# Optimization experiments

Measured on AMD Instinct MI355X. Metric: run time of the kernel, lower is better.

Reference implementation:

```python
import jax, jax.numpy as jnp
import numpy as np

EPS = 1e-5

def _layernorm(x, gamma, beta):
    mu = jnp.mean(x, axis=-1, keepdims=True)
    var = jnp.mean(jnp.square(x - mu), axis=-1, keepdims=True)
    return (x - mu) * jax.lax.rsqrt(var + EPS) * gamma + beta

def setup_inputs() -> dict:
    key = jax.random.key(0)
    kx, kw = jax.random.split(key)
    N, D, BIT = 65536, 1024, 64
    X = jax.random.normal(kx, (N, D), dtype=jnp.float32)
    # xavier_uniform with gain=0.5 for weight [BIT, D]
    limit = 0.5 * np.sqrt(6.0 / (D + BIT))
    W = jax.random.uniform(kw, (BIT, D), minval=-limit, maxval=limit, dtype=jnp.float32)
    b = jnp.zeros((BIT,), dtype=jnp.float32)
    ln1_g = jnp.ones((D,), dtype=jnp.float32)
    ln1_b = jnp.zeros((D,), dtype=jnp.float32)
    ln2_g = jnp.ones((BIT,), dtype=jnp.float32)
    ln2_b = jnp.zeros((BIT,), dtype=jnp.float32)
    return {"X": X, "W": W, "b": b, "ln1_g": ln1_g, "ln1_b": ln1_b, "ln2_g": ln2_g, "ln2_b": ln2_b}

def reference(X, W, b, ln1_g, ln1_b, ln2_g, ln2_b):
    # LayerNorm -> Linear -> LayerNorm
    xn = _layernorm(X, ln1_g, ln1_b)                       # [N, D]
    logits = jnp.einsum('nd,bd->nb', xn, W) + b            # [N, BIT]
    logits = _layernorm(logits, ln2_g, ln2_b)
    # mean-center over batch, tanh, sign-binarize
    logits = logits - jnp.mean(logits, axis=0, keepdims=True)
    H = jnp.tanh(0.5 * logits)
    B = jnp.where(H >= 0.0, jnp.int8(1), jnp.int8(-1))
    return H, B
```

## Files before the change

kernel.cpp:

```cpp
#include <hip/hip_runtime.h>
#include <stdint.h>

#define N_ROWS 65536
#define D_IN   1024
#define NBIT   64
#define LN_EPS 1e-5f

typedef __attribute__((ext_vector_type(8))) _Float16 f16x8;
typedef __attribute__((ext_vector_type(4))) float f32x4;

__device__ __forceinline__ void gload_lds16(const void* g, void* l) {
    __builtin_amdgcn_global_load_lds(
        (const __attribute__((address_space(1))) uint32_t*)g,
        (__attribute__((address_space(3))) uint32_t*)l, 16, 0, 0);
}

__device__ __forceinline__ f32x4 ntload4(const float* p) {
    return __builtin_nontemporal_load((const f32x4*)p);
}

__device__ __forceinline__ f32x4 mfma16(f16x8 a, f16x8 b, f32x4 c) {
    return __builtin_amdgcn_mfma_f32_16x16x32_f16(a, b, c, 0, 0, 0);
}

__device__ __forceinline__ void do_tstep(f32x4 x0, f32x4 x1,
        const _Float16* bhp, f32x4* acc_h, f32x4* acc_m, f32x4* acc_ll,
        float& sum, float& sumsq) {
    float xs[8] = {x0[0], x0[1], x0[2], x0[3], x1[0], x1[1], x1[2], x1[3]};
    f16x8 ahi, alo;
#pragma unroll
    for (int j = 0; j < 8; ++j) {
        float xv = xs[j];
        sum += xv;
        sumsq = fmaf(xv, xv, sumsq);
        _Float16 h = (_Float16)xv;
        ahi[j] = h;
        alo[j] = (_Float16)((xv - (float)h) * 2048.0f);
    }
#pragma unroll
    for (int nt = 0; nt < 4; ++nt) {
        f16x8 bh = *(const f16x8*)(bhp + nt * 512);
        f16x8 bl = *(const f16x8*)(bhp + 4096 + nt * 512);
        acc_h[nt]  = mfma16(ahi, bh, acc_h[nt]);
        acc_m[nt]  = mfma16(ahi, bl, acc_m[nt]);
        acc_m[nt]  = mfma16(alo, bh, acc_m[nt]);
        acc_ll[nt] = mfma16(alo, bl, acc_ll[nt]);
    }
}

__global__ void prep_kernel(const float* __restrict__ W, const float* __restrict__ bias,
                            const float* __restrict__ g1, const float* __restrict__ b1,
                            _Float16* __restrict__ whi, _Float16* __restrict__ wlo,
                            float* __restrict__ u, float* __restrict__ v) {
    int bit = blockIdx.x;
    int t   = threadIdx.x;
    int nt  = bit >> 4, bl = bit & 15;
    float su = 0.f, sv = 0.f;
    for (int d = t; d < D_IN; d += 256) {
        float w  = W[bit * D_IN + d];
        float gw = w * g1[d];
        su += gw;
        sv += w * b1[d];
        int kt = d >> 5, gg = (d >> 3) & 3, j = d & 7;
        size_t idx = (((size_t)(kt * 4 + nt)) * 64 + gg * 16 + bl) * 8 + j;
        _Float16 h = (_Float16)gw;
        whi[idx] = h;
        wlo[idx] = (_Float16)((gw - (float)h) * 2048.0f);
    }
    __shared__ float s1[256], s2[256];
    s1[t] = su; s2[t] = sv;
    __syncthreads();
    for (int off = 128; off > 0; off >>= 1) {
        if (t < off) { s1[t] += s1[t + off]; s2[t] += s2[t + off]; }
        __syncthreads();
    }
    if (t == 0) { u[bit] = s1[0]; v[bit] = s2[0] + bias[bit]; }
}

__global__ void __launch_bounds__(1024) main_kernel(
        const float* __restrict__ X,
        const _Float16* __restrict__ whi, const _Float16* __restrict__ wlo,
        const float* __restrict__ u, const float* __restrict__ v,
        const float* __restrict__ g2, const float* __restrict__ b2,
        float* __restrict__ L, float* __restrict__ P) {
    __shared__ _Float16 lw[2][8192];
    int tid  = threadIdx.x;
    int wid  = tid >> 6, lane = tid & 63;
    int g    = lane >> 4, r16 = lane & 15;
    int row_base = blockIdx.x * 256 + wid * 16;

    const float* xrow = X + (size_t)(row_base + r16) * D_IN + g * 8;

    const _Float16* gsrc = ((wid & 8) ? wlo : whi) + (wid & 7) * 512 + (size_t)lane * 8;
    const int ldst = ((wid & 8) ? 4096 : 0) + (wid & 7) * 512;

#define STAGEW(cc, buf) gload_lds16(gsrc + (size_t)(cc) * 4096, &lw[buf][ldst])

    f32x4 acc_h0[4], acc_h1[4], acc_m[4], acc_ll[4];
#pragma unroll
    for (int nt = 0; nt < 4; ++nt) {
        acc_h0[nt] = (f32x4){0.f, 0.f, 0.f, 0.f};
        acc_h1[nt] = (f32x4){0.f, 0.f, 0.f, 0.f};
        acc_m[nt]  = (f32x4){0.f, 0.f, 0.f, 0.f};
        acc_ll[nt] = (f32x4){0.f, 0.f, 0.f, 0.f};
    }
    float sum = 0.f, sumsq = 0.f;

    STAGEW(0, 0);
    __syncthreads();

    for (int c = 0; c < 16; ++c) {
        if (c < 15) STAGEW(c + 1, (c + 1) & 1);
        int t = c * 2;
        f32x4 x00 = ntload4(xrow + t * 32);
        f32x4 x01 = ntload4(xrow + t * 32 + 4);
        f32x4 x10 = ntload4(xrow + t * 32 + 32);
        f32x4 x11 = ntload4(xrow + t * 32 + 36);
        const _Float16* bhp = &lw[c & 1][0] + lane * 8;
        do_tstep(x00, x01, bhp,        acc_h0, acc_m, acc_ll, sum, sumsq);
        do_tstep(x10, x11, bhp + 2048, acc_h1, acc_m, acc_ll, sum, sumsq);
        __syncthreads();
    }

    sum   += __shfl_xor(sum, 16);   sum   += __shfl_xor(sum, 32);
    sumsq += __shfl_xor(sumsq, 16); sumsq += __shfl_xor(sumsq, 32);
    float mu   = sum * (1.f / 1024.f);
    float var  = sumsq * (1.f / 1024.f) - mu * mu;
    float rstd = rsqrtf(var + LN_EPS);

    float uv[4], vv[4], g2v[4], b2v[4];
#pragma unroll
    for (int nt = 0; nt < 4; ++nt) {
        int bitc = nt * 16 + r16;
        uv[nt] = u[bitc]; vv[nt] = v[bitc]; g2v[nt] = g2[bitc]; b2v[nt] = b2[bitc];
    }
    float mu_m[4], rs_m[4];
#pragma unroll
    for (int reg = 0; reg < 4; ++reg) {
        int m = g * 4 + reg;
        mu_m[reg] = __shfl(mu, m);
        rs_m[reg] = __shfl(rstd, m);
    }

    float lg[4][4];
#pragma unroll
    for (int nt = 0; nt < 4; ++nt)
#pragma unroll
        for (int reg = 0; reg < 4; ++reg) {
            float dot = (acc_h0[nt][reg] + acc_h1[nt][reg])
                      + acc_m[nt][reg] * (1.0f / 2048.0f)
                      + acc_ll[nt][reg] * (1.0f / 4194304.0f);
            lg[nt][reg] = rs_m[reg] * dot - rs_m[reg] * mu_m[reg] * uv[nt] + vv[nt];
        }

#pragma unroll
    for (int reg = 0; reg < 4; ++reg) {
        float s1 = lg[0][reg] + lg[1][reg] + lg[2][reg] + lg[3][reg];
        float s2 = lg[0][reg]*lg[0][reg] + lg[1][reg]*lg[1][reg]
                 + lg[2][reg]*lg[2][reg] + lg[3][reg]*lg[3][reg];
#pragma unroll
        for (int m = 1; m <= 8; m <<= 1) {
            s1 += __shfl_xor(s1, m);
            s2 += __shfl_xor(s2, m);
        }
        float mean = s1 * (1.f / 64.f);
        float va   = s2 * (1.f / 64.f) - mean * mean;
        float rs2  = rsqrtf(va + LN_EPS);
#pragma unroll
        for (int nt = 0; nt < 4; ++nt)
            lg[nt][reg] = (lg[nt][reg] - mean) * rs2 * g2v[nt] + b2v[nt];
    }

#pragma unroll
    for (int reg = 0; reg < 4; ++reg) {
        size_t row = (size_t)(row_base + g * 4 + reg);
#pragma unroll
        for (int nt = 0; nt < 4; ++nt)
            __builtin_nontemporal_store(lg[nt][reg], &L[row * 64 + nt * 16 + r16]);
    }

#pragma unroll
    for (int nt = 0; nt < 4; ++nt) {
        float cs = lg[nt][0] + lg[nt][1] + lg[nt][2] + lg[nt][3];
        cs += __shfl_xor(cs, 16);
        cs += __shfl_xor(cs, 32);
        if (g == 0)
            P[(size_t)(nt * 16 + r16) * 4096 + blockIdx.x * 16 + wid] = cs;
    }
#undef STAGEW
}

__global__ void reduce_kernel(const float* __restrict__ P, float* __restrict__ cm) {
    int bit = blockIdx.x, t = threadIdx.x;
    float s = 0.f;
    for (int p = t; p < 4096; p += 256) s += P[(size_t)bit * 4096 + p];
    __shared__ float sh[256];
    sh[t] = s;
    __syncthreads();
    for (int off = 128; off > 0; off >>= 1) {
        if (t < off) sh[t] += sh[t + off];
        __syncthreads();
    }
    if (t == 0) cm[bit] = sh[0] * (1.f / (float)N_ROWS);
}

__global__ void final_kernel(const float* __restrict__ L, const float* __restrict__ cm,
                             float* __restrict__ out) {
    __shared__ float cms[64];
    if (threadIdx.x < 64) cms[threadIdx.x] = cm[threadIdx.x];
    __syncthreads();
    const f32x4* L4 = (const f32x4*)L;
    f32x4* H4 = (f32x4*)out;
    f32x4* B4 = (f32x4*)(out + (size_t)N_ROWS * NBIT);
    int total = N_ROWS * NBIT / 4;
    for (int i = blockIdx.x * blockDim.x + threadIdx.x; i < total;
         i += gridDim.x * blockDim.x) {
        f32x4 x = __builtin_nontemporal_load(&L4[i]);
        int bb = (i & 15) * 4;
        f32x4 h, bo;
#pragma unroll
        for (int j = 0; j < 4; ++j) {
            h[j]  = tanhf(0.5f * (x[j] - cms[bb + j]));
            bo[j] = h[j] >= 0.f ? 1.f : -1.f;
        }
        __builtin_nontemporal_store(h, &H4[i]);
        __builtin_nontemporal_store(bo, &B4[i]);
    }
}

extern "C" void kernel_launch(void* const* d_in, const int* in_sizes, int n_in,
                              void* d_out, int out_size, void* d_ws, size_t ws_size,
                              hipStream_t stream) {
    (void)in_sizes; (void)n_in; (void)out_size; (void)ws_size;
    const float* X  = (const float*)d_in[0];
    const float* W  = (const float*)d_in[1];
    const float* bb = (const float*)d_in[2];
    const float* g1 = (const float*)d_in[3];
    const float* b1 = (const float*)d_in[4];
    const float* g2 = (const float*)d_in[5];
    const float* b2 = (const float*)d_in[6];

    char* ws = (char*)d_ws;
    _Float16* whi = (_Float16*)ws;
    _Float16* wlo = (_Float16*)(ws + 131072);
    float* u  = (float*)(ws + 262144);
    float* v  = (float*)(ws + 266240);
    float* P  = (float*)(ws + 270336);
    float* cm = (float*)(ws + 270336 + 64 * 4096 * 4);

    float* out = (float*)d_out;
    float* L   = out + (size_t)N_ROWS * NBIT;

    prep_kernel<<<64, 256, 0, stream>>>(W, bb, g1, b1, whi, wlo, u, v);
    main_kernel<<<256, 1024, 0, stream>>>(X, whi, wlo, u, v, g2, b2, L, P);
    reduce_kernel<<<64, 256, 0, stream>>>(P, cm);
    final_kernel<<<2048, 256, 0, stream>>>(L, cm, out);
}
```

Measured before the change: 100.6 us.

## Shrink main blocks to 256 threads, deepen K chunks, use fast tanh

The main kernel moves from 1024-thread blocks over 256 rows to 256-thread blocks over 64 rows, launched as 1024 blocks. Each K chunk now covers 128 columns, with the weight staging tile doubled and each wave issuing eight LDS loads per stage. Nontemporal loads and stores of X and L become ordinary cached accesses, so L may stay in cache for the final pass. The final kernel replaces tanhf with a cubic polynomial for small arguments and __expf otherwise, cutting transcendental cost at some accuracy loss near the switch point. The trade-off is that each block now re-stages the full weight matrix for a quarter as many rows.

Result: faster. 91.87 us (-8.6%).

```diff
diff --git a/kernel.cpp b/kernel.cpp
--- a/kernel.cpp
+++ b/kernel.cpp
@@ -13,10 +13,6 @@
     __builtin_amdgcn_global_load_lds(
         (const __attribute__((address_space(1))) uint32_t*)g,
         (__attribute__((address_space(3))) uint32_t*)l, 16, 0, 0);
-}
-
-__device__ __forceinline__ f32x4 ntload4(const float* p) {
-    return __builtin_nontemporal_load((const f32x4*)p);
 }
 
 __device__ __forceinline__ f32x4 mfma16(f16x8 a, f16x8 b, f32x4 c) {
@@ -40,7 +36,7 @@
 #pragma unroll
     for (int nt = 0; nt < 4; ++nt) {
         f16x8 bh = *(const f16x8*)(bhp + nt * 512);
-        f16x8 bl = *(const f16x8*)(bhp + 4096 + nt * 512);
+        f16x8 bl = *(const f16x8*)(bhp + 8192 + nt * 512);
         acc_h[nt]  = mfma16(ahi, bh, acc_h[nt]);
         acc_m[nt]  = mfma16(ahi, bl, acc_m[nt]);
         acc_m[nt]  = mfma16(alo, bh, acc_m[nt]);
@@ -77,24 +73,30 @@
     if (t == 0) { u[bit] = s1[0]; v[bit] = s2[0] + bias[bit]; }
 }
 
-__global__ void __launch_bounds__(1024) main_kernel(
+__global__ void __launch_bounds__(256) main_kernel(
         const float* __restrict__ X,
         const _Float16* __restrict__ whi, const _Float16* __restrict__ wlo,
         const float* __restrict__ u, const float* __restrict__ v,
         const float* __restrict__ g2, const float* __restrict__ b2,
         float* __restrict__ L, float* __restrict__ P) {
-    __shared__ _Float16 lw[2][8192];
+    __shared__ _Float16 lw[2][16384];
     int tid  = threadIdx.x;
     int wid  = tid >> 6, lane = tid & 63;
     int g    = lane >> 4, r16 = lane & 15;
-    int row_base = blockIdx.x * 256 + wid * 16;
+    int row_base = blockIdx.x * 64 + wid * 16;
 
     const float* xrow = X + (size_t)(row_base + r16) * D_IN + g * 8;
 
-    const _Float16* gsrc = ((wid & 8) ? wlo : whi) + (wid & 7) * 512 + (size_t)lane * 8;
-    const int ldst = ((wid & 8) ? 4096 : 0) + (wid & 7) * 512;
-
-#define STAGEW(cc, buf) gload_lds16(gsrc + (size_t)(cc) * 4096, &lw[buf][ldst])
+    const _Float16* gsrc = ((wid & 2) ? wlo : whi) + (wid & 1) * 4096 + (size_t)lane * 8;
+    const int ldst = ((wid & 2) ? 8192 : 0) + (wid & 1) * 4096;
+
+#define STAGEW(cc, buf) do {                                                  \
+        const _Float16* gs_ = gsrc + (size_t)(cc) * 8192;                     \
+        _Float16* ld_ = &lw[buf][ldst];                                       \
+        _Pragma("unroll")                                                     \
+        for (int r = 0; r < 8; ++r)                                           \
+            gload_lds16(gs_ + r * 512, ld_ + r * 512);                        \
+    } while (0)
 
     f32x4 acc_h0[4], acc_h1[4], acc_m[4], acc_ll[4];
 #pragma unroll
@@ -109,16 +111,21 @@
     STAGEW(0, 0);
     __syncthreads();
 
-    for (int c = 0; c < 16; ++c) {
-        if (c < 15) STAGEW(c + 1, (c + 1) & 1);
-        int t = c * 2;
-        f32x4 x00 = ntload4(xrow + t * 32);
-        f32x4 x01 = ntload4(xrow + t * 32 + 4);
-        f32x4 x10 = ntload4(xrow + t * 32 + 32);
-        f32x4 x11 = ntload4(xrow + t * 32 + 36);
+    for (int c = 0; c < 8; ++c) {
+        if (c < 7) STAGEW(c + 1, (c + 1) & 1);
+        const float* xp = xrow + c * 128;
+        f32x4 xv[8];
+#pragma unroll
+        for (int t2 = 0; t2 < 4; ++t2) {
+            xv[2 * t2]     = *(const f32x4*)(xp + t2 * 32);
+            xv[2 * t2 + 1] = *(const f32x4*)(xp + t2 * 32 + 4);
+        }
         const _Float16* bhp = &lw[c & 1][0] + lane * 8;
-        do_tstep(x00, x01, bhp,        acc_h0, acc_m, acc_ll, sum, sumsq);
-        do_tstep(x10, x11, bhp + 2048, acc_h1, acc_m, acc_ll, sum, sumsq);
+#pragma unroll
+        for (int t2 = 0; t2 < 4; ++t2) {
+            do_tstep(xv[2 * t2], xv[2 * t2 + 1], bhp + t2 * 2048,
+                     (t2 & 1) ? acc_h1 : acc_h0, acc_m, acc_ll, sum, sumsq);
+        }
         __syncthreads();
     }
 
@@ -176,7 +183,7 @@
         size_t row = (size_t)(row_base + g * 4 + reg);
 #pragma unroll
         for (int nt = 0; nt < 4; ++nt)
-            __builtin_nontemporal_store(lg[nt][reg], &L[row * 64 + nt * 16 + r16]);
+            L[row * 64 + nt * 16 + r16] = lg[nt][reg];
     }
 
 #pragma unroll
@@ -185,7 +192,7 @@
         cs += __shfl_xor(cs, 16);
         cs += __shfl_xor(cs, 32);
         if (g == 0)
-            P[(size_t)(nt * 16 + r16) * 4096 + blockIdx.x * 16 + wid] = cs;
+            P[(size_t)(nt * 16 + r16) * 4096 + blockIdx.x * 4 + wid] = cs;
     }
 #undef STAGEW
 }
@@ -215,13 +222,19 @@
     int total = N_ROWS * NBIT / 4;
     for (int i = blockIdx.x * blockDim.x + threadIdx.x; i < total;
          i += gridDim.x * blockDim.x) {
-        f32x4 x = __builtin_nontemporal_load(&L4[i]);
+        f32x4 x = L4[i];
         int bb = (i & 15) * 4;
         f32x4 h, bo;
 #pragma unroll
         for (int j = 0; j < 4; ++j) {
-            h[j]  = tanhf(0.5f * (x[j] - cms[bb + j]));
-            bo[j] = h[j] >= 0.f ? 1.f : -1.f;
+            float y  = 0.5f * (x[j] - cms[bb + j]);
+            float y2 = y * y;
+            float poly = y * fmaf(y2, fmaf(y2, 2.f / 15.f, -1.f / 3.f), 1.f);
+            float e  = __expf(2.f * y);
+            float ef = 1.f - 2.f / (e + 1.f);
+            float hv = (fabsf(y) < 0.5f) ? poly : ef;
+            h[j]  = hv;
+            bo[j] = hv >= 0.f ? 1.f : -1.f;
         }
         __builtin_nontemporal_store(h, &H4[i]);
         __builtin_nontemporal_store(bo, &B4[i]);
@@ -252,7 +265,7 @@
     float* L   = out + (size_t)N_ROWS * NBIT;
 
     prep_kernel<<<64, 256, 0, stream>>>(W, bb, g1, b1, whi, wlo, u, v);
-    main_kernel<<<256, 1024, 0, stream>>>(X, whi, wlo, u, v, g2, b2, L, P);
+    main_kernel<<<1024, 256, 0, stream>>>(X, whi, wlo, u, v, g2, b2, L, P);
     reduce_kernel<<<64, 256, 0, stream>>>(P, cm);
     final_kernel<<<2048, 256, 0, stream>>>(L, cm, out);
 }
```
